# Performance work log

Measured on AMD Instinct MI355X. Metric: run time of the kernel, lower is better.

The kernel has to match this reference:

```python
import jax, jax.numpy as jnp
import numpy as np

D = 128      # feature dim
H = 8        # heads
DH = D // H  # dim per head
N = 100000   # nodes
E = 600000   # edges
BN_EPS = 1e-5


def _bn(x, g, b, m, v):
    # BatchNorm1d in eval mode (running stats)
    return (x - m) * jax.lax.rsqrt(v + BN_EPS) * g + b


def setup_inputs() -> dict:
    key = jax.random.key(0)
    ks = jax.random.split(key, 32)
    s = 1.0 / np.sqrt(D)
    inp = {
        "x": jax.random.normal(ks[0], (N, D), jnp.float32),
        "edge_index": jax.random.randint(ks[1], (2, E), 0, N, jnp.int64),
        # type embeddings (1 node type, 1 edge type)
        "nt_emb": jax.random.normal(ks[2], (1, D), jnp.float32),
        "et_emb": jax.random.normal(ks[3], (1, D), jnp.float32),
        # merge_node_edge_attr: Linear(2D,D) -> BN -> ReLU -> Linear(D,D)
        "mW1": jax.random.normal(ks[4], (2 * D, D), jnp.float32) * s,
        "mb1": jnp.zeros((D,), jnp.float32),
        "m_g": jnp.ones((D,), jnp.float32),
        "m_b": jnp.zeros((D,), jnp.float32),
        "m_m": jax.random.normal(ks[5], (D,), jnp.float32) * 0.1,
        "m_v": jax.random.uniform(ks[6], (D,), jnp.float32, 0.5, 1.5),
        "mW2": jax.random.normal(ks[7], (D, D), jnp.float32) * s,
        "mb2": jnp.zeros((D,), jnp.float32),
        # residual projection (no bias)
        "resW": jax.random.normal(ks[8], (D, D), jnp.float32) * s,
        # attention projections
        "qW": jax.random.normal(ks[9], (D, D), jnp.float32) * s,
        "qb": jnp.zeros((D,), jnp.float32),
        "kW": jax.random.normal(ks[10], (D, D), jnp.float32) * s,
        "kb": jnp.zeros((D,), jnp.float32),
        "vW": jax.random.normal(ks[11], (D, D), jnp.float32) * s,
        "vb": jnp.zeros((D,), jnp.float32),
        # output mlp: Linear -> BN -> LeakyReLU -> Linear
        "oW1": jax.random.normal(ks[12], (D, D), jnp.float32) * s,
        "ob1": jnp.zeros((D,), jnp.float32),
        "o_g": jnp.ones((D,), jnp.float32),
        "o_b": jnp.zeros((D,), jnp.float32),
        "o_m": jax.random.normal(ks[13], (D,), jnp.float32) * 0.1,
        "o_v": jax.random.uniform(ks[14], (D,), jnp.float32, 0.5, 1.5),
        "oW2": jax.random.normal(ks[15], (D, D), jnp.float32) * s,
        "ob2": jnp.zeros((D,), jnp.float32),
    }
    return inp


def reference(x, edge_index, nt_emb, et_emb, mW1, mb1, m_g, m_b, m_m, m_v, mW2, mb2,
              resW, qW, qb, kW, kb, vW, vb, oW1, ob1, o_g, o_b, o_m, o_v, oW2, ob2):
    src = edge_index[0]
    dst = edge_index[1]
    n_nodes = x.shape[0]
    e = edge_index.shape[1]

    # GraphNodeEdgeAttr: edge attrs are constant per edge type; with one node
    # type, edge_attr[0] == edge_attr[1] == merge(cat[node_emb, edge_emb]).
    merged = jnp.concatenate([nt_emb[0], et_emb[0]])          # [2D]
    h = jax.nn.relu(_bn(merged @ mW1 + mb1, m_g, m_b, m_m, m_v))
    ea = h @ mW2 + mb2                                        # [D], broadcasts per edge

    # edge_update: per-edge multi-head attention scores
    x_j = x[src]                                              # [E, D] source feats
    x_i = x[dst]                                              # [E, D] target feats
    q = ((x_j + ea) @ qW + qb).reshape(e, H, DH) / jnp.sqrt(jnp.float32(DH))
    k = ((x_i + ea) @ kW + kb).reshape(e, H, DH)
    msg = (x_j @ vW + vb).reshape(e, H, DH)
    scores = jnp.sum(q * k, axis=2)                           # [E, H]

    # segment softmax keyed by source node index
    smax = jax.ops.segment_max(scores, src, num_segments=n_nodes)
    ex = jnp.exp(scores - smax[src])
    ssum = jax.ops.segment_sum(ex, src, num_segments=n_nodes)
    alpha = ex / ssum[src]                                    # [E, H]

    # message + scatter-add aggregation to destination nodes
    weighted = (msg * alpha[:, :, None]).reshape(e, H * DH)   # [E, D]
    aggr = jax.ops.segment_sum(weighted, dst, num_segments=n_nodes)  # [N, D]

    res = x @ resW
    z = aggr + res
    out = jax.nn.leaky_relu(_bn(z @ oW1 + ob1, o_g, o_b, o_m, o_v)) @ oW2 + ob2
    return out
```

## Files before the change

### kernel.cpp

```cpp
#include <hip/hip_runtime.h>

#define BN_EPS 1e-5f
#define SCAN_CHUNK 1024
#define BM 128

typedef __attribute__((ext_vector_type(8))) short s16x8;
typedef __attribute__((ext_vector_type(8))) ushort u16x8;
typedef __attribute__((ext_vector_type(4))) float f32x4;

__device__ __forceinline__ ushort f2bf_rne(float f)
{
    unsigned u = __builtin_bit_cast(unsigned, f);
    return (ushort)((u + 0x7fffu + ((u >> 16) & 1u)) >> 16);
}

__device__ __forceinline__ float bf2f(ushort u)
{
    return __builtin_bit_cast(float, (unsigned)u << 16);
}

__global__ __launch_bounds__(128) void k_ea(
    const float* __restrict__ nt, const float* __restrict__ et,
    const float* __restrict__ mW1, const float* __restrict__ mb1,
    const float* __restrict__ m_g, const float* __restrict__ m_b,
    const float* __restrict__ m_m, const float* __restrict__ m_v,
    const float* __restrict__ mW2, const float* __restrict__ mb2,
    const float* __restrict__ qW, const float* __restrict__ qb,
    const float* __restrict__ kW, const float* __restrict__ kb,
    float* __restrict__ eaq, float* __restrict__ eak)
{
    __shared__ float merged[256];
    __shared__ float h[128];
    __shared__ float sea[128];
    const int t = threadIdx.x;
    merged[t]       = nt[t];
    merged[128 + t] = et[t];
    __syncthreads();
    float acc = mb1[t];
    for (int i = 0; i < 256; ++i) acc = fmaf(merged[i], mW1[i * 128 + t], acc);
    acc = (acc - m_m[t]) * rsqrtf(m_v[t] + BN_EPS) * m_g[t] + m_b[t];
    h[t] = acc > 0.f ? acc : 0.f;
    __syncthreads();
    float acc2 = mb2[t];
    for (int k = 0; k < 128; ++k) acc2 = fmaf(h[k], mW2[k * 128 + t], acc2);
    sea[t] = acc2;
    __syncthreads();
    float aq = qb[t], ak = kb[t];
    for (int k = 0; k < 128; ++k) {
        const float e = sea[k];
        aq = fmaf(e, qW[k * 128 + t], aq);
        ak = fmaf(e, kW[k * 128 + t], ak);
    }
    eaq[t] = aq;
    eak[t] = ak;
}

__device__ __forceinline__ void split_store(float w, ushort* __restrict__ base,
                                            int j, int k)
{
    unsigned u = __builtin_bit_cast(unsigned, w);
    unsigned hi = (u + 0x7fffu + ((u >> 16) & 1u)) >> 16;
    float hif = __builtin_bit_cast(float, hi << 16);
    float res = w - hif;
    unsigned lo = __builtin_bit_cast(unsigned, res) >> 16;
    base[j * 128 + k]         = (ushort)hi;
    base[16384 + j * 128 + k] = (ushort)lo;
}

__global__ __launch_bounds__(128) void k_prep3(
    const float* __restrict__ W0, const float* __restrict__ W1,
    const float* __restrict__ W2, ushort* __restrict__ P)
{
    const int j = blockIdx.x;
    const int m = blockIdx.y;
    const int k = threadIdx.x;
    const float* W = (m == 0) ? W0 : (m == 1) ? W1 : W2;
    split_store(W[k * 128 + j], P + (size_t)m * 32768, j, k);
}

__global__ __launch_bounds__(128) void k_prep_out(
    const float* __restrict__ resW, const float* __restrict__ oW1,
    const float* __restrict__ oW2, ushort* __restrict__ P)
{
    __shared__ float col[128];
    const int j = blockIdx.x;
    const int m = blockIdx.y;
    const int k = threadIdx.x;
    float w;
    if (m == 0) {
        col[k] = oW1[k * 128 + j];
        __syncthreads();
        float acc = 0.f;
        for (int i = 0; i < 128; ++i) acc = fmaf(resW[k * 128 + i], col[i], acc);
        w = acc;
    } else {
        const float* W = (m == 1) ? oW1 : oW2;
        w = W[k * 128 + j];
    }
    split_store(w, P + (size_t)m * 32768, j, k);
}

template <int NT>
__device__ __forceinline__ void stage_w(const ushort* __restrict__ wpl,
                                        ushort* __restrict__ sw, int tid)
{
    const uint4* src = (const uint4*)wpl;
#pragma unroll
    for (int it = 0; it < 4096 / NT; ++it) {
        const int idx = it * NT + tid;
        const uint4 v = src[idx];
        const int plane = idx >> 11;
        const int rr = (idx >> 4) & 127;
        const int cb = (idx & 15) << 4;
        const int byteoff = ((rr * 256 + cb) ^ ((rr & 7) << 4));
        *(uint4*)((char*)sw + plane * 32768 + byteoff) = v;
    }
}

template <int NT>
__device__ __forceinline__ void stage_w1(const ushort* __restrict__ wpl,
                                         ushort* __restrict__ sw, int tid)
{
    const uint4* src = (const uint4*)wpl;
#pragma unroll
    for (int it = 0; it < 2048 / NT; ++it) {
        const int idx = it * NT + tid;
        const uint4 v = src[idx];
        const int rr = idx >> 4;
        const int cb = (idx & 15) << 4;
        const int byteoff = ((rr * 256 + cb) ^ ((rr & 7) << 4));
        *(uint4*)((char*)sw + byteoff) = v;
    }
}

__device__ __forceinline__ void split_row(const float* __restrict__ row, int g,
                                          s16x8* ah, s16x8* al)
{
#pragma unroll
    for (int ks = 0; ks < 4; ++ks) {
        const float* ap = row + ks * 32 + g * 8;
        const float4 a0 = *(const float4*)(ap);
        const float4 a1 = *(const float4*)(ap + 4);
        float av[8] = {a0.x, a0.y, a0.z, a0.w, a1.x, a1.y, a1.z, a1.w};
#pragma unroll
        for (int j = 0; j < 8; ++j) {
            const unsigned u = __builtin_bit_cast(unsigned, av[j]);
            ah[ks][j] = (short)(u >> 16);
            const float hif = __builtin_bit_cast(float, u & 0xffff0000u);
            const float res = av[j] - hif;
            al[ks][j] = (short)(__builtin_bit_cast(unsigned, res) >> 16);
        }
    }
}

template <int CT>
__device__ __forceinline__ void mm_core(const float* __restrict__ Arow,
                                        const ushort* __restrict__ sw,
                                        int g, int r16, int ct0, f32x4* acc)
{
#pragma unroll
    for (int ks = 0; ks < 4; ++ks) {
        const float* ap = Arow + ks * 32 + g * 8;
        const float4 a0 = *(const float4*)(ap);
        const float4 a1 = *(const float4*)(ap + 4);
        float av[8] = {a0.x, a0.y, a0.z, a0.w, a1.x, a1.y, a1.z, a1.w};
        s16x8 ahi, alo;
#pragma unroll
        for (int j = 0; j < 8; ++j) {
            const unsigned u = __builtin_bit_cast(unsigned, av[j]);
            ahi[j] = (short)(u >> 16);
            const float hif = __builtin_bit_cast(float, u & 0xffff0000u);
            const float res = av[j] - hif;
            alo[j] = (short)(__builtin_bit_cast(unsigned, res) >> 16);
        }
        const int koff = ks * 64 + g * 16;
#pragma unroll
        for (int ct = 0; ct < CT; ++ct) {
            const int row = (ct0 + ct) * 16 + r16;
            const int byteoff = ((row * 256 + koff) ^ ((row & 7) << 4));
            const s16x8 bhi = *(const s16x8*)((const char*)sw + byteoff);
            const s16x8 blo = *(const s16x8*)((const char*)sw + 32768 + byteoff);
            acc[ct] = __builtin_amdgcn_mfma_f32_16x16x32_bf16(ahi, bhi, acc[ct], 0, 0, 0);
            acc[ct] = __builtin_amdgcn_mfma_f32_16x16x32_bf16(ahi, blo, acc[ct], 0, 0, 0);
            acc[ct] = __builtin_amdgcn_mfma_f32_16x16x32_bf16(alo, bhi, acc[ct], 0, 0, 0);
        }
    }
}

template <int CT>
__device__ __forceinline__ void mm_pass2(const s16x8* ah, const s16x8* al,
                                         const ushort* __restrict__ sw,
                                         int g, int r16, int ct0, f32x4* acc)
{
#pragma unroll
    for (int ks = 0; ks < 4; ++ks) {
        const int koff = ks * 64 + g * 16;
#pragma unroll
        for (int ct = 0; ct < CT; ++ct) {
            const int row = (ct0 + ct) * 16 + r16;
            const int byteoff = ((row * 256 + koff) ^ ((row & 7) << 4));
            const s16x8 b = *(const s16x8*)((const char*)sw + byteoff);
            acc[ct] = __builtin_amdgcn_mfma_f32_16x16x32_bf16(ah[ks], b, acc[ct], 0, 0, 0);
            acc[ct] = __builtin_amdgcn_mfma_f32_16x16x32_bf16(al[ks], b, acc[ct], 0, 0, 0);
        }
    }
}

template <int CT>
__device__ __forceinline__ void mm_pass1(const s16x8* a,
                                         const ushort* __restrict__ sw,
                                         int g, int r16, int ct0, f32x4* acc)
{
#pragma unroll
    for (int ks = 0; ks < 4; ++ks) {
        const int koff = ks * 64 + g * 16;
#pragma unroll
        for (int ct = 0; ct < CT; ++ct) {
            const int row = (ct0 + ct) * 16 + r16;
            const int byteoff = ((row * 256 + koff) ^ ((row & 7) << 4));
            const s16x8 b = *(const s16x8*)((const char*)sw + byteoff);
            acc[ct] = __builtin_amdgcn_mfma_f32_16x16x32_bf16(a[ks], b, acc[ct], 0, 0, 0);
        }
    }
}

__global__ __launch_bounds__(1024, 8) void k_mm_qkv(
    const float* __restrict__ x, const ushort* __restrict__ planes,
    const float* __restrict__ eaq, const float* __restrict__ eak,
    const float* __restrict__ vb,
    ushort* __restrict__ Q16, ushort* __restrict__ K16, ushort* __restrict__ V16, int N)
{
    __shared__ ushort sw[2 * 128 * 128];
    const int tid = threadIdx.x;
    const int sel = blockIdx.x;
    stage_w<1024>(planes + (size_t)sel * 32768, sw, tid);
    __syncthreads();

    const int wave = tid >> 6, lane = tid & 63;
    const int g = lane >> 4, r16 = lane & 15;
    const int wr = wave & 7, wc = wave >> 3;
    const int ct0 = wc * 4;
    const int n0 = blockIdx.y * BM;
    const int arow = wr * 16 + r16;
    int nA = n0 + arow; if (nA >= N) nA = N - 1;

    f32x4 acc[4];
#pragma unroll
    for (int ct = 0; ct < 4; ++ct) acc[ct] = (f32x4){0.f, 0.f, 0.f, 0.f};
    mm_core<4>(x + (size_t)nA * 128, sw, g, r16, ct0, acc);
    __syncthreads();

    ushort* vbuf = (ushort*)sw;
    const float* bias = (sel == 0) ? eaq : (sel == 1) ? eak : vb;
    ushort* Obf       = (sel == 0) ? Q16 : (sel == 1) ? K16 : V16;
    const float scale = (sel == 0) ? 0.25f : 1.0f;
#pragma unroll
    for (int ct = 0; ct < 4; ++ct) {
        const int c = (ct0 + ct) * 16 + r16;
        const float bc = bias[c];
#pragma unroll
        for (int r = 0; r < 4; ++r) {
            const int nrel = wr * 16 + g * 4 + r;
            vbuf[nrel * 128 + c] = f2bf_rne((acc[ct][r] + bc) * scale);
        }
    }
    __syncthreads();
    const int row = tid >> 3;
    const int col = (tid & 7) * 16;
    if (n0 + row < N) {
        const uint4* src = (const uint4*)(vbuf + row * 128 + col);
        const uint4 v0 = src[0], v1 = src[1];
        uint4* dst = (uint4*)(Obf + (size_t)(n0 + row) * 128 + col);
        dst[0] = v0; dst[1] = v1;
    }
}

__global__ __launch_bounds__(512, 4) void k_out4(
    const float* __restrict__ x, const ushort* __restrict__ Po,
    const float* __restrict__ aggr, const float* __restrict__ ob1,
    const float* __restrict__ o_m, const float* __restrict__ o_v,
    const float* __restrict__ o_g, const float* __restrict__ o_b,
    const float* __restrict__ ob2, float* __restrict__ out, int N)
{
    __shared__ ushort lds[2 * 128 * 128];
    ushort* sw = lds;
    ushort* tb = lds + 16384;
    const int tid = threadIdx.x;
    const int wave = tid >> 6, lane = tid & 63;
    const int g = lane >> 4, r16 = lane & 15;
    const int wr = wave;
    const int n0 = blockIdx.x * 128;
    const int arow = wr * 16 + r16;
    int nA = n0 + arow; if (nA >= N) nA = N - 1;

    s16x8 ah[4], al[4];
    split_row(x + (size_t)nA * 128, g, ah, al);

    f32x4 acc[8];
#pragma unroll
    for (int ct = 0; ct < 8; ++ct) acc[ct] = (f32x4){0.f, 0.f, 0.f, 0.f};

    stage_w1<512>(Po, sw, tid); __syncthreads();
    mm_pass2<8>(ah, al, sw, g, r16, 0, acc); __syncthreads();
    stage_w1<512>(Po + 16384, sw, tid); __syncthreads();
    mm_pass1<8>(ah, sw, g, r16, 0, acc); __syncthreads();

    split_row(aggr + (size_t)nA * 128, g, ah, al);
    stage_w1<512>(Po + 32768, sw, tid); __syncthreads();
    mm_pass2<8>(ah, al, sw, g, r16, 0, acc); __syncthreads();
    stage_w1<512>(Po + 49152, sw, tid); __syncthreads();
    mm_pass1<8>(ah, sw, g, r16, 0, acc); __syncthreads();

#pragma unroll
    for (int ct = 0; ct < 8; ++ct) {
        const int c = ct * 16 + r16;
        const float bc = ob1[c];
        const float rs = rsqrtf(o_v[c] + BN_EPS);
        const float mm = o_m[c], gg = o_g[c], bb = o_b[c];
#pragma unroll
        for (int r = 0; r < 4; ++r) {
            const int nrel = wr * 16 + g * 4 + r;
            float u = acc[ct][r] + bc;
            u = (u - mm) * rs * gg + bb;
            u = u > 0.f ? u : 0.01f * u;
            const int byteoff = ((nrel * 256 + c * 2) ^ ((nrel & 7) << 4));
            *(ushort*)((char*)tb + byteoff) = f2bf_rne(u);
        }
    }
    stage_w1<512>(Po + 65536, sw, tid);
    __syncthreads();

    s16x8 ta[4];
#pragma unroll
    for (int ks = 0; ks < 4; ++ks) {
        const int byteoff = ((arow * 256 + ks * 64 + g * 16) ^ ((arow & 7) << 4));
        ta[ks] = *(const s16x8*)((const char*)tb + byteoff);
    }
#pragma unroll
    for (int ct = 0; ct < 8; ++ct) acc[ct] = (f32x4){0.f, 0.f, 0.f, 0.f};
    mm_pass1<8>(ta, sw, g, r16, 0, acc);
    __syncthreads();
    stage_w1<512>(Po + 81920, sw, tid); __syncthreads();
    mm_pass1<8>(ta, sw, g, r16, 0, acc);
    __syncthreads();

    float* fbuf = (float*)lds;
#pragma unroll
    for (int ct = 0; ct < 8; ++ct) {
        const int c = ct * 16 + r16;
        const float bc = ob2[c];
#pragma unroll
        for (int r = 0; r < 4; ++r) {
            const int nrel = wr * 16 + g * 4 + r;
            const int byteoff = (nrel * 512 + c * 4) ^ ((nrel & 7) << 4);
            *(float*)((char*)fbuf + byteoff) = acc[ct][r] + bc;
        }
    }
    __syncthreads();
    const float4* fb4 = (const float4*)fbuf;
#pragma unroll
    for (int it = 0; it < 8; ++it) {
        const int idx4 = it * 512 + tid;
        const int row = idx4 >> 5;
        const int n = n0 + row;
        if (n < N)
            *(float4*)(out + (size_t)n * 128 + (idx4 & 31) * 4) =
                fb4[row * 32 + ((idx4 & 31) ^ (row & 7))];
    }
}

__global__ __launch_bounds__(256) void k_edge1csr(
    const int* __restrict__ esrc, const int* __restrict__ row_start,
    const int* __restrict__ deg, const ushort* __restrict__ Q16,
    const ushort* __restrict__ K16, float* __restrict__ exp_,
    float* __restrict__ ssum, int N)
{
    const int tid = threadIdx.x;
    const int n = blockIdx.x * 4 + (tid >> 6);
    if (n >= N) return;
    const int lane = tid & 63;
    const int sub = lane >> 3;
    const int h = lane & 7;
    const int c0 = h * 16;
    const int rs = row_start[n];
    const int dg = deg[n];
    const u16x8 ka = *(const u16x8*)(K16 + (size_t)n * 128 + c0);
    const u16x8 kb = *(const u16x8*)(K16 + (size_t)n * 128 + c0 + 8);
    float kr[16];
#pragma unroll
    for (int i = 0; i < 8; ++i) { kr[i] = bf2f(ka[i]); kr[8 + i] = bf2f(kb[i]); }
    for (int j = sub; j < dg; j += 8) {
        const int idx = rs + j;
        const int s = esrc[idx];
        const u16x8 qa = *(const u16x8*)(Q16 + (size_t)s * 128 + c0);
        const u16x8 qb_ = *(const u16x8*)(Q16 + (size_t)s * 128 + c0 + 8);
        float p = 0.f;
#pragma unroll
        for (int i = 0; i < 8; ++i) {
            p = fmaf(bf2f(qa[i]),  kr[i],     p);
            p = fmaf(bf2f(qb_[i]), kr[8 + i], p);
        }
        const float v = __expf(p);
        exp_[(size_t)idx * 8 + h] = v;
        unsafeAtomicAdd(&ssum[(size_t)s * 8 + h], v);
    }
}

__global__ __launch_bounds__(256) void k_rsum(float* __restrict__ ssum, int M)
{
    const int i = blockIdx.x * 256 + threadIdx.x;
    if (i < M) ssum[i] = 1.0f / ssum[i];
}

__global__ __launch_bounds__(256) void k_hist(const int* __restrict__ ei,
                                              int* __restrict__ deg, int E)
{
    const int e = blockIdx.x * 256 + threadIdx.x;
    if (e < E) atomicAdd(&deg[ei[E + e]], 1);
}

__global__ __launch_bounds__(256) void k_scan_partial(const int* __restrict__ deg,
                                                      int* __restrict__ part, int N)
{
    __shared__ int sd[256];
    const int b = blockIdx.x, t = threadIdx.x;
    const int base = b * SCAN_CHUNK + t * 4;
    int s = 0;
#pragma unroll
    for (int i = 0; i < 4; ++i) { const int idx = base + i; if (idx < N) s += deg[idx]; }
    sd[t] = s; __syncthreads();
    for (int off = 128; off > 0; off >>= 1) {
        if (t < off) sd[t] += sd[t + off];
        __syncthreads();
    }
    if (t == 0) part[b] = sd[0];
}

__global__ __launch_bounds__(256) void k_scan_top(int* __restrict__ part, int nb)
{
    __shared__ int sd[256];
    const int t = threadIdx.x;
    const int orig = (t < nb) ? part[t] : 0;
    sd[t] = orig;
    __syncthreads();
    for (int off = 1; off < 256; off <<= 1) {
        const int v = (t >= off) ? sd[t - off] : 0;
        __syncthreads();
        sd[t] += v;
        __syncthreads();
    }
    if (t < nb) part[t] = sd[t] - orig;
}

__global__ __launch_bounds__(256) void k_scan_final(const int* __restrict__ deg,
                                                    const int* __restrict__ part,
                                                    int* __restrict__ row_start,
                                                    int* __restrict__ cursor, int N)
{
    __shared__ int ts[256];
    const int b = blockIdx.x, t = threadIdx.x;
    const int base = b * SCAN_CHUNK + t * 4;
    int v[4]; int s = 0;
#pragma unroll
    for (int i = 0; i < 4; ++i) { const int idx = base + i; v[i] = (idx < N) ? deg[idx] : 0; s += v[i]; }
    ts[t] = s; __syncthreads();
    for (int off = 1; off < 256; off <<= 1) {
        const int vv = (t >= off) ? ts[t - off] : 0;
        __syncthreads();
        ts[t] += vv;
        __syncthreads();
    }
    int run = part[b] + ((t > 0) ? ts[t - 1] : 0);
#pragma unroll
    for (int i = 0; i < 4; ++i) {
        const int idx = base + i;
        if (idx < N) { row_start[idx] = run; cursor[idx] = run; run += v[i]; }
    }
}

__global__ __launch_bounds__(256) void k_scatter(const int* __restrict__ ei,
                                                 int* __restrict__ cursor,
                                                 int* __restrict__ esrc, int E)
{
    const int e = blockIdx.x * 256 + threadIdx.x;
    if (e < E) {
        const int pos = atomicAdd(&cursor[ei[E + e]], 1);
        esrc[pos] = ei[e];
    }
}

__global__ __launch_bounds__(256) void k_aggr(
    const int* __restrict__ esrc, const int* __restrict__ row_start,
    const int* __restrict__ deg, const ushort* __restrict__ V16,
    const float* __restrict__ exp_, const float* __restrict__ rsum,
    float* __restrict__ aggr, int N)
{
    const int tid = threadIdx.x;
    const int n = blockIdx.x * 4 + (tid >> 6);
    if (n >= N) return;
    const int lane = tid & 63;
    const int sub = lane >> 3;
    const int h = lane & 7;
    const int c0 = h * 16;
    const int rs = row_start[n];
    const int dg = deg[n];
    float acc[16];
#pragma unroll
    for (int i = 0; i < 16; ++i) acc[i] = 0.f;
    for (int j = sub; j < dg; j += 8) {
        const int idx = rs + j;
        const int s = esrc[idx];
        const float a = exp_[(size_t)idx * 8 + h] * rsum[(size_t)s * 8 + h];
        const u16x8 v0 = *(const u16x8*)(V16 + (size_t)s * 128 + c0);
        const u16x8 v1 = *(const u16x8*)(V16 + (size_t)s * 128 + c0 + 8);
#pragma unroll
        for (int i = 0; i < 8; ++i) {
            acc[i]     = fmaf(bf2f(v0[i]), a, acc[i]);
            acc[8 + i] = fmaf(bf2f(v1[i]), a, acc[8 + i]);
        }
    }
#pragma unroll
    for (int i = 0; i < 16; ++i) {
        acc[i] += __shfl_xor(acc[i], 8, 64);
        acc[i] += __shfl_xor(acc[i], 16, 64);
        acc[i] += __shfl_xor(acc[i], 32, 64);
    }
    if (sub == 0) {
#pragma unroll
        for (int q = 0; q < 4; ++q) {
            float4 o = make_float4(acc[q * 4], acc[q * 4 + 1],
                                   acc[q * 4 + 2], acc[q * 4 + 3]);
            *(float4*)(aggr + (size_t)n * 128 + c0 + q * 4) = o;
        }
    }
}

extern "C" void kernel_launch(void* const* d_in, const int* in_sizes, int n_in,
                              void* d_out, int out_size, void* d_ws, size_t ws_size,
                              hipStream_t stream)
{
    const float* x    = (const float*)d_in[0];
    const int*   ei   = (const int*)d_in[1];
    const float* nt   = (const float*)d_in[2];
    const float* et   = (const float*)d_in[3];
    const float* mW1  = (const float*)d_in[4];
    const float* mb1  = (const float*)d_in[5];
    const float* m_g  = (const float*)d_in[6];
    const float* m_b  = (const float*)d_in[7];
    const float* m_m  = (const float*)d_in[8];
    const float* m_v  = (const float*)d_in[9];
    const float* mW2  = (const float*)d_in[10];
    const float* mb2  = (const float*)d_in[11];
    const float* resW = (const float*)d_in[12];
    const float* qW   = (const float*)d_in[13];
    const float* qb   = (const float*)d_in[14];
    const float* kW   = (const float*)d_in[15];
    const float* kb   = (const float*)d_in[16];
    const float* vW   = (const float*)d_in[17];
    const float* vb   = (const float*)d_in[18];
    const float* oW1  = (const float*)d_in[19];
    const float* ob1  = (const float*)d_in[20];
    const float* o_g  = (const float*)d_in[21];
    const float* o_b  = (const float*)d_in[22];
    const float* o_m  = (const float*)d_in[23];
    const float* o_v  = (const float*)d_in[24];
    const float* oW2  = (const float*)d_in[25];
    const float* ob2  = (const float*)d_in[26];
    float* out = (float*)d_out;

    const int N = in_sizes[0] / 128;
    const int E = in_sizes[1] / 2;

    float* ws   = (float*)d_ws;
    float* eaq  = ws;
    float* eak  = ws + 128;
    float* Q    = ws + 256;
    float* K    = Q + (size_t)N * 128;
    float* V    = K + (size_t)N * 128;
    float* exp_ = V + (size_t)N * 128;
    float* ssum = exp_ + (size_t)E * 8;
    int* deg       = (int*)(ssum + (size_t)N * 8);
    int* row_start = deg + N;
    int* cursor    = row_start + N;
    int* part      = cursor + N;
    int* esrc      = part + 256;
    float* aggr = Q;
    ushort* Q16 = (ushort*)Q;
    ushort* K16 = (ushort*)K;
    ushort* V16 = (ushort*)V;
    ushort* Pq = (ushort*)ssum;
    ushort* Po = (ushort*)exp_;

    const int nbm  = (N + BM - 1) / BM;
    const int nbo  = (N + 127) / 128;
    const int nbsc = (N + SCAN_CHUNK - 1) / SCAN_CHUNK;

    k_prep3<<<dim3(128, 3), 128, 0, stream>>>(qW, kW, vW, Pq);
    k_ea<<<1, 128, 0, stream>>>(nt, et, mW1, mb1, m_g, m_b, m_m, m_v, mW2, mb2,
                                qW, qb, kW, kb, eaq, eak);
    k_mm_qkv<<<dim3(3, nbm), 1024, 0, stream>>>(x, Pq, eaq, eak, vb, Q16, K16, V16, N);

    hipMemsetAsync(ssum, 0, (size_t)N * 8 * sizeof(float), stream);
    hipMemsetAsync(deg, 0, (size_t)N * sizeof(int), stream);

    k_hist<<<(E + 255) / 256, 256, 0, stream>>>(ei, deg, E);
    k_scan_partial<<<nbsc, 256, 0, stream>>>(deg, part, N);
    k_scan_top<<<1, 256, 0, stream>>>(part, nbsc);
    k_scan_final<<<nbsc, 256, 0, stream>>>(deg, part, row_start, cursor, N);
    k_scatter<<<(E + 255) / 256, 256, 0, stream>>>(ei, cursor, esrc, E);

    k_edge1csr<<<(N + 3) / 4, 256, 0, stream>>>(esrc, row_start, deg, Q16, K16, exp_, ssum, N);
    k_rsum<<<(N * 8 + 255) / 256, 256, 0, stream>>>(ssum, N * 8);
    k_aggr<<<(N + 3) / 4, 256, 0, stream>>>(esrc, row_start, deg, V16, exp_, ssum, aggr, N);

    k_prep_out<<<dim3(128, 3), 128, 0, stream>>>(resW, oW1, oW2, Po);
    k_out4<<<nbo, 512, 0, stream>>>(x, Po, aggr, ob1, o_m, o_v, o_g, o_b, ob2, out, N);
}
```

Measured before the change: 437.9 us.

## Double-buffer weight staging in output MLP, swizzle QKV epilogue LDS, reorder grid

The output kernel now uses two LDS buffers, so the next weight plane loads while the current one feeds MFMAs, and some barriers are dropped. The QKV epilogue writes to a XOR-swizzled LDS layout to avoid bank conflicts on the column-strided bf16 stores. The QKV grid is swapped so node blocks vary fastest and each weight matrix is staged by consecutive blocks. The risk is that the tanh-buffer reuse ordering in the output kernel is subtle, and the extra prefetch raises register pressure.

Result: no change. 437.1 us (-0.2%).

```diff
diff --git a/kernel.cpp b/kernel.cpp
--- a/kernel.cpp
+++ b/kernel.cpp
@@ -232,7 +232,7 @@
 {
     __shared__ ushort sw[2 * 128 * 128];
     const int tid = threadIdx.x;
-    const int sel = blockIdx.x;
+    const int sel = blockIdx.y;
     stage_w<1024>(planes + (size_t)sel * 32768, sw, tid);
     __syncthreads();
 
@@ -240,7 +240,7 @@
     const int g = lane >> 4, r16 = lane & 15;
     const int wr = wave & 7, wc = wave >> 3;
     const int ct0 = wc * 4;
-    const int n0 = blockIdx.y * BM;
+    const int n0 = blockIdx.x * BM;
     const int arow = wr * 16 + r16;
     int nA = n0 + arow; if (nA >= N) nA = N - 1;
 
@@ -261,15 +261,17 @@
 #pragma unroll
         for (int r = 0; r < 4; ++r) {
             const int nrel = wr * 16 + g * 4 + r;
-            vbuf[nrel * 128 + c] = f2bf_rne((acc[ct][r] + bc) * scale);
+            const int byteoff = (nrel * 256 + c * 2) ^ ((nrel & 7) << 4);
+            *(ushort*)((char*)vbuf + byteoff) = f2bf_rne((acc[ct][r] + bc) * scale);
         }
     }
     __syncthreads();
     const int row = tid >> 3;
     const int col = (tid & 7) * 16;
     if (n0 + row < N) {
-        const uint4* src = (const uint4*)(vbuf + row * 128 + col);
-        const uint4 v0 = src[0], v1 = src[1];
+        const int xv = (row & 7) << 4;
+        const uint4 v0 = *(const uint4*)((const char*)vbuf + ((row * 256 + col * 2) ^ xv));
+        const uint4 v1 = *(const uint4*)((const char*)vbuf + ((row * 256 + col * 2 + 16) ^ xv));
         uint4* dst = (uint4*)(Obf + (size_t)(n0 + row) * 128 + col);
         dst[0] = v0; dst[1] = v1;
     }
@@ -283,8 +285,8 @@
     const float* __restrict__ ob2, float* __restrict__ out, int N)
 {
     __shared__ ushort lds[2 * 128 * 128];
-    ushort* sw = lds;
-    ushort* tb = lds + 16384;
+    ushort* buf0 = lds;
+    ushort* buf1 = lds + 16384;
     const int tid = threadIdx.x;
     const int wave = tid >> 6, lane = tid & 63;
     const int g = lane >> 4, r16 = lane & 15;
@@ -300,16 +302,21 @@
 #pragma unroll
     for (int ct = 0; ct < 8; ++ct) acc[ct] = (f32x4){0.f, 0.f, 0.f, 0.f};
 
-    stage_w1<512>(Po, sw, tid); __syncthreads();
-    mm_pass2<8>(ah, al, sw, g, r16, 0, acc); __syncthreads();
-    stage_w1<512>(Po + 16384, sw, tid); __syncthreads();
-    mm_pass1<8>(ah, sw, g, r16, 0, acc); __syncthreads();
-
+    stage_w1<512>(Po, buf0, tid);
+    __syncthreads();
+    stage_w1<512>(Po + 16384, buf1, tid);
+    mm_pass2<8>(ah, al, buf0, g, r16, 0, acc);
+    __syncthreads();
+    stage_w1<512>(Po + 32768, buf0, tid);
+    mm_pass1<8>(ah, buf1, g, r16, 0, acc);
+    __syncthreads();
     split_row(aggr + (size_t)nA * 128, g, ah, al);
-    stage_w1<512>(Po + 32768, sw, tid); __syncthreads();
-    mm_pass2<8>(ah, al, sw, g, r16, 0, acc); __syncthreads();
-    stage_w1<512>(Po + 49152, sw, tid); __syncthreads();
-    mm_pass1<8>(ah, sw, g, r16, 0, acc); __syncthreads();
+    stage_w1<512>(Po + 49152, buf1, tid);
+    mm_pass2<8>(ah, al, buf0, g, r16, 0, acc);
+    __syncthreads();
+    stage_w1<512>(Po + 65536, buf0, tid);
+    mm_pass1<8>(ah, buf1, g, r16, 0, acc);
+    __syncthreads();
 
 #pragma unroll
     for (int ct = 0; ct < 8; ++ct) {
@@ -324,24 +331,24 @@
             u = (u - mm) * rs * gg + bb;
             u = u > 0.f ? u : 0.01f * u;
             const int byteoff = ((nrel * 256 + c * 2) ^ ((nrel & 7) << 4));
-            *(ushort*)((char*)tb + byteoff) = f2bf_rne(u);
-        }
-    }
-    stage_w1<512>(Po + 65536, sw, tid);
+            *(ushort*)((char*)buf1 + byteoff) = f2bf_rne(u);
+        }
+    }
     __syncthreads();
 
     s16x8 ta[4];
 #pragma unroll
     for (int ks = 0; ks < 4; ++ks) {
         const int byteoff = ((arow * 256 + ks * 64 + g * 16) ^ ((arow & 7) << 4));
-        ta[ks] = *(const s16x8*)((const char*)tb + byteoff);
+        ta[ks] = *(const s16x8*)((const char*)buf1 + byteoff);
     }
 #pragma unroll
     for (int ct = 0; ct < 8; ++ct) acc[ct] = (f32x4){0.f, 0.f, 0.f, 0.f};
-    mm_pass1<8>(ta, sw, g, r16, 0, acc);
-    __syncthreads();
-    stage_w1<512>(Po + 81920, sw, tid); __syncthreads();
-    mm_pass1<8>(ta, sw, g, r16, 0, acc);
+    mm_pass1<8>(ta, buf0, g, r16, 0, acc);
+    __syncthreads();
+    stage_w1<512>(Po + 81920, buf1, tid);
+    __syncthreads();
+    mm_pass1<8>(ta, buf1, g, r16, 0, acc);
     __syncthreads();
 
     float* fbuf = (float*)lds;
@@ -598,7 +605,7 @@
     k_prep3<<<dim3(128, 3), 128, 0, stream>>>(qW, kW, vW, Pq);
     k_ea<<<1, 128, 0, stream>>>(nt, et, mW1, mb1, m_g, m_b, m_m, m_v, mW2, mb2,
                                 qW, qb, kW, kb, eaq, eak);
-    k_mm_qkv<<<dim3(3, nbm), 1024, 0, stream>>>(x, Pq, eaq, eak, vb, Q16, K16, V16, N);
+    k_mm_qkv<<<dim3(nbm, 3), 1024, 0, stream>>>(x, Pq, eaq, eak, vb, Q16, K16, V16, N);
 
     hipMemsetAsync(ssum, 0, (size_t)N * 8 * sizeof(float), stream);
     hipMemsetAsync(deg, 0, (size_t)N * sizeof(int), stream);
```
